# Kernel tuning notes

Measured on AMD Instinct MI355X. Metric: run time of the kernel, lower is better.

Reference implementation:

```python
import jax, jax.numpy as jnp
import numpy as np

HEAD_SIZE = 64
BLOCK_SIZE = 4096
BATCH = 4


def setup_inputs() -> dict:
    key = jax.random.key(0)
    kx, kk, kq, kv = jax.random.split(key, 4)
    x = jax.random.normal(kx, (BATCH, BLOCK_SIZE, HEAD_SIZE), dtype=jnp.float32)
    s = HEAD_SIZE ** -0.5  # ~ torch default linear init scale
    Wk = jax.random.uniform(kk, (HEAD_SIZE, HEAD_SIZE), jnp.float32, -s, s)
    Wq = jax.random.uniform(kq, (HEAD_SIZE, HEAD_SIZE), jnp.float32, -s, s)
    Wv = jax.random.uniform(kv, (HEAD_SIZE, HEAD_SIZE), jnp.float32, -s, s)
    return {"x": x, "Wk": Wk, "Wq": Wq, "Wv": Wv}


def reference(x, Wk, Wq, Wv):
    # x: [B, T, C]; W*: [C, C] stored torch-style (out, in) -> y = x @ W.T
    B, T, C = x.shape
    k = x @ Wk.T  # [B, T, C]
    q = x @ Wq.T
    v = x @ Wv.T
    scores = jnp.einsum('btc,bsc->bts', q, k) * (C ** -0.5)  # [B, T, T]
    causal = jnp.tril(jnp.ones((T, T), dtype=bool))
    scores = jnp.where(causal, scores, -jnp.inf)
    weights = jax.nn.softmax(scores, axis=-1)
    out = jnp.einsum('bts,bsc->btc', weights, v)  # [B, T, C]
    return out
```

## Files before the change

### kernel.cpp

```cpp
#include <hip/hip_runtime.h>
#include <hip/hip_bf16.h>

typedef unsigned short u16;
typedef unsigned int u32;
typedef __bf16 bf16x8_t __attribute__((ext_vector_type(8)));
typedef float f32x4_t __attribute__((ext_vector_type(4)));

constexpr int Bb = 4;
constexpr int Tt = 4096;
constexpr int Dd = 64;
constexpr float QSCALE = 0.18033688011112042f;

__device__ __forceinline__ u16 f2bf(float f) {
  unsigned int u = __builtin_bit_cast(unsigned int, f);
  return (u16)((u + 0x7fffu + ((u >> 16) & 1u)) >> 16);
}
__device__ __forceinline__ u32 pk2(float a, float b) {
  return (u32)f2bf(a) | ((u32)f2bf(b) << 16);
}
__device__ __forceinline__ u32 pkt(float a, float b) {
  const u32 ua = __builtin_bit_cast(u32, a);
  const u32 ub = __builtin_bit_cast(u32, b);
  return (ua >> 16) | (ub & 0xFFFF0000u);
}
__device__ __forceinline__ bf16x8_t ld16(const u16* p) {
  int4 v = *(const int4*)p;
  return __builtin_bit_cast(bf16x8_t, v);
}
__device__ __forceinline__ f32x4_t mfma16(bf16x8_t a, bf16x8_t b, f32x4_t c) {
  return __builtin_amdgcn_mfma_f32_16x16x32_bf16(a, b, c, 0, 0, 0);
}

__global__ __launch_bounds__(256) void HeadV1_proj(
    const float* __restrict__ x, const float* __restrict__ Wk,
    const float* __restrict__ Wq, const float* __restrict__ Wv,
    u16* __restrict__ qS, u16* __restrict__ kS, u16* __restrict__ vS)
{
  __shared__ u16 xl[64][72];
  __shared__ u16 Wl[3][64][72];
  __shared__ u16 ylds[64][72];

  const int t = threadIdx.x;
  const int w = t >> 6, lane = t & 63, l15 = lane & 15, quad = lane >> 4;
  const int r0 = blockIdx.x * 64;
  const int b  = r0 >> 12;
  const int kt = (r0 & 4095) >> 6;
  const long tilebase = ((long)(b * 64 + kt)) * 4096;

  {
    const float* srcs[4] = {x + (long)r0 * 64, Wk, Wq, Wv};
    u16* dstl[4] = {&xl[0][0], &Wl[0][0][0], &Wl[1][0][0], &Wl[2][0][0]};
    #pragma unroll
    for (int mm = 0; mm < 4; mm++) {
      const float* s = srcs[mm];
      u16* d = dstl[mm];
      #pragma unroll
      for (int i = 0; i < 4; i++) {
        const int f4 = i * 256 + t;
        const int row = f4 >> 4, c4 = f4 & 15;
        float4 v = ((const float4*)(s + row * 64))[c4];
        uint2 pk;
        pk.x = pk2(v.x, v.y);
        pk.y = pk2(v.z, v.w);
        *(uint2*)(d + row * 72 + c4 * 4) = pk;
      }
    }
  }
  __syncthreads();

  bf16x8_t xf[2];
  #pragma unroll
  for (int kh = 0; kh < 2; kh++)
    xf[kh] = ld16(&xl[w * 16 + l15][kh * 32 + quad * 8]);

  u16* dsts[3];
  dsts[0] = kS + tilebase; dsts[1] = qS + tilebase; dsts[2] = vS + tilebase;

  #pragma unroll
  for (int m = 0; m < 3; m++) {
    float vals[4][4];
    #pragma unroll
    for (int g = 0; g < 4; g++) {
      f32x4_t acc = {0.f, 0.f, 0.f, 0.f};
      #pragma unroll
      for (int kh = 0; kh < 2; kh++) {
        bf16x8_t wf = ld16(&Wl[m][g * 16 + l15][kh * 32 + quad * 8]);
        acc = mfma16(xf[kh], wf, acc);
      }
      #pragma unroll
      for (int r = 0; r < 4; r++)
        vals[g][r] = (m == 1) ? acc[r] * QSCALE : acc[r];
    }
    #pragma unroll
    for (int g = 0; g < 4; g++)
      #pragma unroll
      for (int r = 0; r < 4; r++)
        ylds[w * 16 + quad * 4 + r][g * 16 + l15] = f2bf(vals[g][r]);
    __syncthreads();
    if (m < 2) {
      #pragma unroll
      for (int kk = 0; kk < 2; kk++) {
        bf16x8_t f = ld16(&ylds[w * 16 + l15][kk * 32 + quad * 8]);
        *(int4*)(dsts[m] + (w * 2 + kk) * 512 + lane * 8) = __builtin_bit_cast(int4, f);
      }
    } else {
      #pragma unroll
      for (int kk = 0; kk < 2; kk++) {
        u16 tmp[8];
        #pragma unroll
        for (int j = 0; j < 8; j++)
          tmp[j] = ylds[kk * 32 + quad * 8 + j][w * 16 + l15];
        *(int4*)(dsts[2] + (kk * 4 + w) * 512 + lane * 8) = *(const int4*)tmp;
      }
    }
    __syncthreads();
  }
}

__global__ __launch_bounds__(1024, 4) void HeadV1_flash(
    const u16* __restrict__ qS, const u16* __restrict__ kS,
    const u16* __restrict__ vS, float* __restrict__ outg)
{
  __shared__ __align__(16) char smem[53248];
  u16  (*pT)[32][36]   = (u16 (*)[32][36])smem;
  float (*chk)[16][33] = (float (*)[16][33])smem;
  float (*stg)[32][68] = (float (*)[32][68])(smem + 33792);
  float (*lst)[32]     = (float (*)[32])(smem + 33792 + 17408);

  const int t    = threadIdx.x;
  const int w    = t >> 6;
  const int lane = t & 63;
  const int l15  = lane & 15;
  const int quad = lane >> 4;

  const int xcd = blockIdx.x & 7;
  const int b   = xcd >> 1;
  const int i   = ((blockIdx.x >> 3) << 1) | (xcd & 1);
  const int j1 = i, j2 = 127 - i;
  const int nk1 = (j1 >> 1) + 1;
  const int nk2 = (j2 >> 1) + 1;
  int n1 = (16 * nk1 + 32) / 65;
  if (n1 < 1) n1 = 1;
  if (n1 > 15) n1 = 15;

  const bool grp2 = (w >= n1);
  const int j   = grp2 ? j2 : j1;
  const int nk  = grp2 ? nk2 : nk1;
  const int str = grp2 ? (16 - n1) : n1;
  const int off = grp2 ? (w - n1) : w;

  const int qt64 = j >> 1;
  const int ql0  = (j & 1) * 32;
  const int qr0  = j * 32;
  const long base = (long)b * Tt * Dd;

  union { u32 u4[4]; bf16x8_t v; } uo;
  uo.u4[0] = uo.u4[1] = uo.u4[2] = uo.u4[3] = 0x3F803F80u;
  const bf16x8_t ones = uo.v;
  const f32x4_t zero4 = {0.f, 0.f, 0.f, 0.f};

  const u16* qtile = qS + ((long)(b * 64 + qt64)) * 4096 + lane * 8;
  bf16x8_t qfrag[2][2];
  #pragma unroll
  for (int ct = 0; ct < 2; ct++)
    #pragma unroll
    for (int kd = 0; kd < 2; kd++)
      qfrag[ct][kd] = ld16(qtile + ((ql0 / 16 + ct) * 2 + kd) * 512);

  f32x4_t O[4][2];
  #pragma unroll
  for (int a = 0; a < 4; a++)
    #pragma unroll
    for (int c = 0; c < 2; c++)
      O[a][c] = zero4;
  f32x4_t Lc[2] = {zero4, zero4};

  for (int kt = off; kt < nk; kt += str) {
    const bool ismask = (kt == nk - 1);
    const int kv0 = kt * 64;
    const u16* ktile = kS + ((long)(b * 64 + kt)) * 4096 + lane * 8;
    const u16* vtile = vS + ((long)(b * 64 + kt)) * 4096 + lane * 8;

    #pragma unroll
    for (int kk = 0; kk < 2; kk++) {
      bf16x8_t vf[4];
      #pragma unroll
      for (int dt = 0; dt < 4; dt++)
        vf[dt] = ld16(vtile + (kk * 4 + dt) * 512);

      #pragma unroll
      for (int rtl = 0; rtl < 2; rtl++) {
        const int rt = kk * 2 + rtl;
        bf16x8_t kf0 = ld16(ktile + (rt * 2 + 0) * 512);
        bf16x8_t kf1 = ld16(ktile + (rt * 2 + 1) * 512);
        #pragma unroll
        for (int ct = 0; ct < 2; ct++) {
          f32x4_t acc = zero4;
          acc = mfma16(kf0, qfrag[ct][0], acc);
          acc = mfma16(kf1, qfrag[ct][1], acc);
          if (ismask) {
            const int kvl = kv0 + rt * 16 + quad * 4;
            const int qi  = qr0 + ct * 16 + l15;
            #pragma unroll
            for (int r = 0; r < 4; r++)
              if (kvl + r > qi) acc[r] = -1e30f;
          }
          const float p0 = __builtin_amdgcn_exp2f(acc[0]);
          const float p1 = __builtin_amdgcn_exp2f(acc[1]);
          const float p2 = __builtin_amdgcn_exp2f(acc[2]);
          const float p3 = __builtin_amdgcn_exp2f(acc[3]);
          uint2 pk;
          pk.x = pkt(p0, p1);
          pk.y = pkt(p2, p3);
          *(uint2*)&pT[w][ct * 16 + l15][rtl * 16 + quad * 4] = pk;
        }
      }
      #pragma unroll
      for (int ct = 0; ct < 2; ct++) {
        bf16x8_t pf = ld16(&pT[w][ct * 16 + l15][quad * 8]);
        #pragma unroll
        for (int dt = 0; dt < 4; dt++)
          O[dt][ct] = mfma16(vf[dt], pf, O[dt][ct]);
        Lc[ct] = mfma16(ones, pf, Lc[ct]);
      }
    }
  }

  if (quad == 0) {
    #pragma unroll
    for (int ct = 0; ct < 2; ct++)
      lst[w][ct * 16 + l15] = Lc[ct][0];
  }
  __syncthreads();

  #pragma unroll
  for (int dt = 0; dt < 4; dt++) {
    #pragma unroll
    for (int ct = 0; ct < 2; ct++)
      #pragma unroll
      for (int r = 0; r < 4; r++)
        chk[w][quad * 4 + r][ct * 16 + l15] = O[dt][ct][r];
    __syncthreads();
    {
      const int jsel = t >> 9, tt = t & 511;
      const int d2 = tt >> 5, q = tt & 31;
      const int lo = jsel ? n1 : 0, hi = jsel ? 16 : n1;
      float s = 0.f;
      for (int w2 = lo; w2 < hi; w2++) s += chk[w2][d2][q];
      stg[jsel][q][dt * 16 + d2] = s;
    }
    __syncthreads();
  }

  {
    const int jsel = t >> 9, tt = t & 511;
    const int q = tt >> 4, dg = tt & 15;
    const int lo = jsel ? n1 : 0, hi = jsel ? 16 : n1;
    float L = 0.f;
    for (int w2 = lo; w2 < hi; w2++) L += lst[w2][q];
    const float invL = 1.0f / L;
    const int jj = jsel ? j2 : j1;
    float4 v = *(const float4*)&stg[jsel][q][dg * 4];
    v.x *= invL; v.y *= invL; v.z *= invL; v.w *= invL;
    *(float4*)(outg + base + (long)(jj * 32 + q) * 64 + dg * 4) = v;
  }
}

extern "C" void kernel_launch(void* const* d_in, const int* in_sizes, int n_in,
                              void* d_out, int out_size, void* d_ws, size_t ws_size,
                              hipStream_t stream) {
  (void)in_sizes; (void)n_in; (void)out_size; (void)ws_size;
  const float* x  = (const float*)d_in[0];
  const float* Wk = (const float*)d_in[1];
  const float* Wq = (const float*)d_in[2];
  const float* Wv = (const float*)d_in[3];
  float* out = (float*)d_out;
  u16* qw  = (u16*)d_ws;
  u16* kw  = qw + (size_t)Bb * Tt * Dd;
  u16* vw  = kw + (size_t)Bb * Tt * Dd;

  HeadV1_proj<<<(Bb * Tt) / 64, 256, 0, stream>>>(x, Wk, Wq, Wv, qw, kw, vw);
  HeadV1_flash<<<256, 1024, 0, stream>>>(qw, kw, vw, out);
}
```

Baseline: 83.78 us.

## Switch flash loop to 32x32x16 MFMA with register-shuffled P and causal half-skip

Replaces the 16x16x32 MFMA tiles with 32x32x16 MFMA for both QK^T and PV. The P operand is now rearranged in registers with cross-half-wave shuffles instead of a round trip through shared memory. The row sum is accumulated with scalar adds on the bf16-truncated probabilities rather than an extra MFMA against a ones vector. On even query tiles it also skips the fully masked second 32-key half of the diagonal tile, and it wraps the PV MFMAs in s_setprio. The aim is fewer instructions, no LDS traffic in the inner loop, and less wasted causal work, at the cost of more registers and more complex fragment index maps.

```diff
diff --git a/kernel.cpp b/kernel.cpp
--- a/kernel.cpp
+++ b/kernel.cpp
@@ -5,6 +5,7 @@
 typedef unsigned int u32;
 typedef __bf16 bf16x8_t __attribute__((ext_vector_type(8)));
 typedef float f32x4_t __attribute__((ext_vector_type(4)));
+typedef float f32x16 __attribute__((ext_vector_type(16)));
 
 constexpr int Bb = 4;
 constexpr int Tt = 4096;
@@ -29,6 +30,9 @@
 }
 __device__ __forceinline__ f32x4_t mfma16(bf16x8_t a, bf16x8_t b, f32x4_t c) {
   return __builtin_amdgcn_mfma_f32_16x16x32_bf16(a, b, c, 0, 0, 0);
+}
+__device__ __forceinline__ f32x16 mfma32(bf16x8_t a, bf16x8_t b, f32x16 c) {
+  return __builtin_amdgcn_mfma_f32_32x32x16_bf16(a, b, c, 0, 0, 0);
 }
 
 __global__ __launch_bounds__(256) void HeadV1_proj(
@@ -121,17 +125,18 @@
     const u16* __restrict__ qS, const u16* __restrict__ kS,
     const u16* __restrict__ vS, float* __restrict__ outg)
 {
-  __shared__ __align__(16) char smem[53248];
-  u16  (*pT)[32][36]   = (u16 (*)[32][36])smem;
-  float (*chk)[16][33] = (float (*)[16][33])smem;
-  float (*stg)[32][68] = (float (*)[32][68])(smem + 33792);
-  float (*lst)[32]     = (float (*)[32])(smem + 33792 + 17408);
+  __shared__ __align__(16) char smem[55296];
+  float (*chk)[16][33]  = (float (*)[16][33])smem;
+  float (*stg)[32][68]  = (float (*)[32][68])(smem + 33792);
+  float (*lst)[2][32]   = (float (*)[2][32])(smem + 51200);
 
   const int t    = threadIdx.x;
   const int w    = t >> 6;
   const int lane = t & 63;
   const int l15  = lane & 15;
-  const int quad = lane >> 4;
+  const int lhb  = lane >> 5;
+  const int l4   = (lane >> 4) & 1;
+  const int q31  = lane & 31;
 
   const int xcd = blockIdx.x & 7;
   const int b   = xcd >> 1;
@@ -154,92 +159,98 @@
   const int qr0  = j * 32;
   const long base = (long)b * Tt * Dd;
 
-  union { u32 u4[4]; bf16x8_t v; } uo;
-  uo.u4[0] = uo.u4[1] = uo.u4[2] = uo.u4[3] = 0x3F803F80u;
-  const bf16x8_t ones = uo.v;
-  const f32x4_t zero4 = {0.f, 0.f, 0.f, 0.f};
-
-  const u16* qtile = qS + ((long)(b * 64 + qt64)) * 4096 + lane * 8;
-  bf16x8_t qfrag[2][2];
-  #pragma unroll
-  for (int ct = 0; ct < 2; ct++)
-    #pragma unroll
-    for (int kd = 0; kd < 2; kd++)
-      qfrag[ct][kd] = ld16(qtile + ((ql0 / 16 + ct) * 2 + kd) * 512);
-
-  f32x4_t O[4][2];
-  #pragma unroll
-  for (int a = 0; a < 4; a++)
-    #pragma unroll
-    for (int c = 0; c < 2; c++)
-      O[a][c] = zero4;
-  f32x4_t Lc[2] = {zero4, zero4};
+  const u16* qt_ = qS + ((long)(b * 64 + qt64)) * 4096;
+  bf16x8_t qfrag[4];
+  #pragma unroll
+  for (int dsl = 0; dsl < 4; dsl++)
+    qfrag[dsl] = ld16(qt_ + (((ql0 >> 4) + l4) * 2 + (dsl >> 1)) * 512
+                          + (((dsl * 2 + lhb) & 3) * 16 + l15) * 8);
+
+  f32x16 O0 = {0.f,0.f,0.f,0.f,0.f,0.f,0.f,0.f,0.f,0.f,0.f,0.f,0.f,0.f,0.f,0.f};
+  f32x16 O1 = O0;
+  float Lp = 0.f;
+
+  const u16* kb = kS + ((long)(b * 64)) * 4096;
+  const u16* vb = vS + ((long)(b * 64)) * 4096;
 
   for (int kt = off; kt < nk; kt += str) {
     const bool ismask = (kt == nk - 1);
-    const int kv0 = kt * 64;
-    const u16* ktile = kS + ((long)(b * 64 + kt)) * 4096 + lane * 8;
-    const u16* vtile = vS + ((long)(b * 64 + kt)) * 4096 + lane * 8;
-
-    #pragma unroll
-    for (int kk = 0; kk < 2; kk++) {
-      bf16x8_t vf[4];
-      #pragma unroll
-      for (int dt = 0; dt < 4; dt++)
-        vf[dt] = ld16(vtile + (kk * 4 + dt) * 512);
-
-      #pragma unroll
-      for (int rtl = 0; rtl < 2; rtl++) {
-        const int rt = kk * 2 + rtl;
-        bf16x8_t kf0 = ld16(ktile + (rt * 2 + 0) * 512);
-        bf16x8_t kf1 = ld16(ktile + (rt * 2 + 1) * 512);
+    const u16* ktile = kb + (long)kt * 4096;
+    const u16* vtile = vb + (long)kt * 4096;
+    const int nh = (ismask && !(j & 1)) ? 1 : 2;
+
+    for (int h2 = 0; h2 < nh; h2++) {
+      bf16x8_t kf[4];
+      #pragma unroll
+      for (int dsl = 0; dsl < 4; dsl++)
+        kf[dsl] = ld16(ktile + ((h2 * 2 + l4) * 2 + (dsl >> 1)) * 512
+                             + (((dsl * 2 + lhb) & 3) * 16 + l15) * 8);
+      bf16x8_t vf[2][2];
+      #pragma unroll
+      for (int ksl = 0; ksl < 2; ksl++)
         #pragma unroll
-        for (int ct = 0; ct < 2; ct++) {
-          f32x4_t acc = zero4;
-          acc = mfma16(kf0, qfrag[ct][0], acc);
-          acc = mfma16(kf1, qfrag[ct][1], acc);
-          if (ismask) {
-            const int kvl = kv0 + rt * 16 + quad * 4;
-            const int qi  = qr0 + ct * 16 + l15;
-            #pragma unroll
-            for (int r = 0; r < 4; r++)
-              if (kvl + r > qi) acc[r] = -1e30f;
-          }
-          const float p0 = __builtin_amdgcn_exp2f(acc[0]);
-          const float p1 = __builtin_amdgcn_exp2f(acc[1]);
-          const float p2 = __builtin_amdgcn_exp2f(acc[2]);
-          const float p3 = __builtin_amdgcn_exp2f(acc[3]);
-          uint2 pk;
-          pk.x = pkt(p0, p1);
-          pk.y = pkt(p2, p3);
-          *(uint2*)&pT[w][ct * 16 + l15][rtl * 16 + quad * 4] = pk;
+        for (int dh = 0; dh < 2; dh++)
+          vf[ksl][dh] = ld16(vtile + (h2 * 4 + dh * 2 + l4) * 512
+                                   + ((ksl * 2 + lhb) * 16 + l15) * 8);
+
+      f32x16 S = {0.f,0.f,0.f,0.f,0.f,0.f,0.f,0.f,0.f,0.f,0.f,0.f,0.f,0.f,0.f,0.f};
+      #pragma unroll
+      for (int dsl = 0; dsl < 4; dsl++)
+        S = mfma32(kf[dsl], qfrag[dsl], S);
+
+      if (ismask && h2 == (j & 1)) {
+        const int kvb = kt * 64 + h2 * 32 + 4 * lhb;
+        const int qi  = qr0 + q31;
+        #pragma unroll
+        for (int r = 0; r < 16; r++) {
+          const int kvg = kvb + (r & 3) + 8 * (r >> 2);
+          if (kvg > qi) S[r] = -1e30f;
         }
       }
-      #pragma unroll
-      for (int ct = 0; ct < 2; ct++) {
-        bf16x8_t pf = ld16(&pT[w][ct * 16 + l15][quad * 8]);
-        #pragma unroll
-        for (int dt = 0; dt < 4; dt++)
-          O[dt][ct] = mfma16(vf[dt], pf, O[dt][ct]);
-        Lc[ct] = mfma16(ones, pf, Lc[ct]);
-      }
-    }
-  }
-
-  if (quad == 0) {
-    #pragma unroll
-    for (int ct = 0; ct < 2; ct++)
-      lst[w][ct * 16 + l15] = Lc[ct][0];
-  }
+
+      float p[16];
+      #pragma unroll
+      for (int r = 0; r < 16; r++) p[r] = __builtin_amdgcn_exp2f(S[r]);
+      #pragma unroll
+      for (int r = 0; r < 16; r++) {
+        const u32 u = __builtin_bit_cast(u32, p[r]) & 0xFFFF0000u;
+        Lp += __builtin_bit_cast(float, u);
+      }
+
+      #pragma unroll
+      for (int ksl = 0; ksl < 2; ksl++) {
+        const u32 a0 = pkt(p[8 * ksl + 0], p[8 * ksl + 1]);
+        const u32 a1 = pkt(p[8 * ksl + 2], p[8 * ksl + 3]);
+        const u32 a2 = pkt(p[8 * ksl + 4], p[8 * ksl + 5]);
+        const u32 a3 = pkt(p[8 * ksl + 6], p[8 * ksl + 7]);
+        const u32 x02 = (u32)__shfl_xor((int)(lhb ? a0 : a2), 32);
+        const u32 x13 = (u32)__shfl_xor((int)(lhb ? a1 : a3), 32);
+        uint4 bw;
+        bw.x = lhb ? x02 : a0;
+        bw.y = lhb ? x13 : a1;
+        bw.z = lhb ? a2 : x02;
+        bw.w = lhb ? a3 : x13;
+        const bf16x8_t Bf = __builtin_bit_cast(bf16x8_t, bw);
+        __builtin_amdgcn_s_setprio(1);
+        O0 = mfma32(vf[ksl][0], Bf, O0);
+        O1 = mfma32(vf[ksl][1], Bf, O1);
+        __builtin_amdgcn_s_setprio(0);
+      }
+    }
+  }
+
+  lst[w][lhb][q31] = Lp;
   __syncthreads();
 
   #pragma unroll
-  for (int dt = 0; dt < 4; dt++) {
-    #pragma unroll
-    for (int ct = 0; ct < 2; ct++)
-      #pragma unroll
-      for (int r = 0; r < 4; r++)
-        chk[w][quad * 4 + r][ct * 16 + l15] = O[dt][ct][r];
+  for (int rr = 0; rr < 4; rr++) {
+    #pragma unroll
+    for (int rs = 0; rs < 8; rs++) {
+      const int dloc = (rs & 3) + 8 * (rs >> 2) + 4 * lhb;
+      const float val = (rr >> 1) ? ((rr & 1) ? O1[8 + rs] : O1[rs])
+                                  : ((rr & 1) ? O0[8 + rs] : O0[rs]);
+      chk[w][dloc][q31] = val;
+    }
     __syncthreads();
     {
       const int jsel = t >> 9, tt = t & 511;
@@ -247,7 +258,7 @@
       const int lo = jsel ? n1 : 0, hi = jsel ? 16 : n1;
       float s = 0.f;
       for (int w2 = lo; w2 < hi; w2++) s += chk[w2][d2][q];
-      stg[jsel][q][dt * 16 + d2] = s;
+      stg[jsel][q][rr * 16 + d2] = s;
     }
     __syncthreads();
   }
@@ -257,7 +268,7 @@
     const int q = tt >> 4, dg = tt & 15;
     const int lo = jsel ? n1 : 0, hi = jsel ? 16 : n1;
     float L = 0.f;
-    for (int w2 = lo; w2 < hi; w2++) L += lst[w2][q];
+    for (int w2 = lo; w2 < hi; w2++) L += lst[w2][0][q] + lst[w2][1][q];
     const float invL = 1.0f / L;
     const int jj = jsel ? j2 : j1;
     float4 v = *(const float4*)&stg[jsel][q][dg * 4];
```

After: 83.13 us. Within noise of the previous version (-0.8%).
